# Performance work log

Measured on AMD Instinct MI355X. Metric: run time of the kernel, lower is better.

## Reference

```python
import jax, jax.numpy as jnp
import numpy as np

N_NODES = 100000
N_EDGES = 1200000
IN_DIM = 64
HID = 64
N_GRAPHS = 512
N_CLASSES = 1
LN_EPS = 1e-5
NORM_EPS = 1e-12


def _layer_norm(x, g, b):
    mu = x.mean(-1, keepdims=True)
    var = ((x - mu) ** 2).mean(-1, keepdims=True)
    return (x - mu) * jax.lax.rsqrt(var + LN_EPS) * g + b


def setup_inputs() -> dict:
    key = jax.random.key(0)
    ks = jax.random.split(key, 20)
    h = jax.random.normal(ks[0], (N_NODES, IN_DIM), jnp.float32)
    src = jax.random.randint(ks[1], (N_EDGES,), 0, N_NODES)
    dst = jax.random.randint(ks[2], (N_EDGES,), 0, N_NODES)
    graph_ids = jnp.sort(jax.random.randint(ks[3], (N_NODES,), 0, N_GRAPHS))
    s1 = 1.0 / np.sqrt(IN_DIM)
    s2 = 1.0 / np.sqrt(HID)
    s3 = 1.0 / np.sqrt(2 * HID)
    return {
        "h": h, "src": src, "dst": dst, "graph_ids": graph_ids,
        "W1": jax.random.normal(ks[4], (IN_DIM, HID), jnp.float32) * s1,
        "b1": jnp.zeros((HID,), jnp.float32),
        "W2": jax.random.normal(ks[5], (HID, HID), jnp.float32) * s2,
        "b2": jnp.zeros((HID,), jnp.float32),
        "g1": jnp.ones((HID,), jnp.float32), "be1": jnp.zeros((HID,), jnp.float32),
        "g2": jnp.ones((HID,), jnp.float32), "be2": jnp.zeros((HID,), jnp.float32),
        "g3": jnp.ones((HID,), jnp.float32), "be3": jnp.zeros((HID,), jnp.float32),
        "g4": jnp.ones((HID,), jnp.float32), "be4": jnp.zeros((HID,), jnp.float32),
        "Wc1": jax.random.normal(ks[6], (2 * HID, HID), jnp.float32) * s3,
        "bc1": jnp.zeros((HID,), jnp.float32),
        "Wc2": jax.random.normal(ks[7], (HID, HID), jnp.float32) * s2,
        "bc2": jnp.zeros((HID,), jnp.float32),
        "Wc3": jax.random.normal(ks[8], (HID, N_CLASSES), jnp.float32) * s2,
        "bc3": jnp.zeros((N_CLASSES,), jnp.float32),
    }


def reference(h, src, dst, graph_ids, W1, b1, W2, b2, g1, be1, g2, be2,
              g3, be3, g4, be4, Wc1, bc1, Wc2, bc2, Wc3, bc3):
    N = N_NODES
    ones_e = jnp.ones((src.shape[0],), jnp.float32)
    # DGL GraphConv norm='both': symmetric degree normalization (clamp 0 -> 1)
    deg_out = jnp.clip(jax.ops.segment_sum(ones_e, src, num_segments=N), 1.0)
    deg_in = jnp.clip(jax.ops.segment_sum(ones_e, dst, num_segments=N), 1.0)
    ns = (deg_out ** -0.5)[:, None]
    nd = (deg_in ** -0.5)[:, None]

    def conv(x, W, b):
        msg = (x * ns)[src]                                  # [E, d] gather
        agg = jax.ops.segment_sum(msg, dst, num_segments=N)  # [N, d] scatter-add
        return (agg * nd) @ W + b

    h1 = jax.nn.relu(_layer_norm(conv(h, W1, b1), g1, be1))
    h1 = jax.nn.relu(_layer_norm(conv(h1, W2, b2), g2, be2))

    # per-graph mean / max pooling (dgl.mean_nodes / dgl.max_nodes)
    ssum = jax.ops.segment_sum(h1, graph_ids, num_segments=N_GRAPHS)
    cnt = jnp.clip(jax.ops.segment_sum(jnp.ones((N,), jnp.float32), graph_ids,
                                       num_segments=N_GRAPHS), 1.0)
    hg = ssum / cnt[:, None]
    hg_max = jax.ops.segment_max(h1, graph_ids, num_segments=N_GRAPHS)

    def l2norm(x):  # F.normalize(p=2, dim=1)
        n = jnp.sqrt((x * x).sum(-1, keepdims=True))
        return x / jnp.maximum(n, NORM_EPS)

    hg = jnp.concatenate([l2norm(hg), l2norm(hg_max)], axis=1)  # [G, 2*HID]
    out = jax.nn.relu(_layer_norm(hg @ Wc1 + bc1, g3, be3))
    out = jax.nn.relu(_layer_norm(out @ Wc2 + bc2, g4, be4))
    return out @ Wc3 + bc3
```

## Files before the change

kernel.cpp:

```cpp
#include <hip/hip_runtime.h>
#include <math.h>

#define HID 64
#define LN_EPS 1e-5f
#define NORM_EPS 1e-12f
#define CHUNK 1024
#define CONV_BLOCKS 2048

__device__ __forceinline__ float wave_sum64(float v) {
#pragma unroll
    for (int o = 32; o > 0; o >>= 1) v += __shfl_xor(v, o, 64);
    return v;
}

__device__ __forceinline__ int lower_bound_dev(const int* __restrict__ a, int n, int key) {
    int lo = 0, hi = n;
    while (lo < hi) {
        int mid = (lo + hi) >> 1;
        if (a[mid] < key) lo = mid + 1; else hi = mid;
    }
    return lo;
}

__global__ __launch_bounds__(256) void count_kernel(const int* __restrict__ src,
                                                    const int* __restrict__ dst,
                                                    int* __restrict__ cnt_out,
                                                    int* __restrict__ cnt_in,
                                                    int E) {
    int e0 = (blockIdx.x * 256 + threadIdx.x) * 4;
    if (e0 + 3 < E) {
        int4 s4 = *reinterpret_cast<const int4*>(src + e0);
        int4 d4 = *reinterpret_cast<const int4*>(dst + e0);
        atomicAdd(&cnt_out[s4.x], 1); atomicAdd(&cnt_out[s4.y], 1);
        atomicAdd(&cnt_out[s4.z], 1); atomicAdd(&cnt_out[s4.w], 1);
        atomicAdd(&cnt_in[d4.x], 1);  atomicAdd(&cnt_in[d4.y], 1);
        atomicAdd(&cnt_in[d4.z], 1);  atomicAdd(&cnt_in[d4.w], 1);
    } else {
        for (int e = e0; e < E; ++e) {
            atomicAdd(&cnt_out[src[e]], 1);
            atomicAdd(&cnt_in[dst[e]], 1);
        }
    }
}

__global__ __launch_bounds__(256) void scan1_kernel(const int* __restrict__ cnt_in,
                                                    const int* __restrict__ cnt_out,
                                                    float* __restrict__ ns,
                                                    float* __restrict__ nd,
                                                    int* __restrict__ cs,
                                                    int* __restrict__ partials,
                                                    int N) {
    __shared__ int wsum[4];
    int t = threadIdx.x;
    int lane = t & 63, wave = t >> 6;
    int base = blockIdx.x * CHUNK + t * 4;
    int v0 = (base + 0 < N) ? cnt_in[base + 0] : 0;
    int v1 = (base + 1 < N) ? cnt_in[base + 1] : 0;
    int v2 = (base + 2 < N) ? cnt_in[base + 2] : 0;
    int v3 = (base + 3 < N) ? cnt_in[base + 3] : 0;

    if (base + 3 < N) {
        int4 co = *reinterpret_cast<const int4*>(cnt_out + base);
        float4 nsv = make_float4(rsqrtf((float)max(co.x, 1)), rsqrtf((float)max(co.y, 1)),
                                 rsqrtf((float)max(co.z, 1)), rsqrtf((float)max(co.w, 1)));
        float4 ndv = make_float4(rsqrtf((float)max(v0, 1)), rsqrtf((float)max(v1, 1)),
                                 rsqrtf((float)max(v2, 1)), rsqrtf((float)max(v3, 1)));
        *reinterpret_cast<float4*>(ns + base) = nsv;
        *reinterpret_cast<float4*>(nd + base) = ndv;
    } else {
        for (int i = base; i < N; ++i) {
            ns[i] = rsqrtf((float)max(cnt_out[i], 1));
            nd[i] = rsqrtf((float)max(cnt_in[i], 1));
        }
    }

    int tsum = v0 + v1 + v2 + v3;
    int x = tsum;
#pragma unroll
    for (int off = 1; off < 64; off <<= 1) {
        int y = __shfl_up(x, off, 64);
        if (lane >= off) x += y;
    }
    if (lane == 63) wsum[wave] = x;
    __syncthreads();
    int waveoff = 0;
    for (int w = 0; w < wave; ++w) waveoff += wsum[w];
    int off0 = waveoff + x - tsum;
    if (base + 0 < N) cs[base + 0] = off0;
    if (base + 1 < N) cs[base + 1] = off0 + v0;
    if (base + 2 < N) cs[base + 2] = off0 + v0 + v1;
    if (base + 3 < N) cs[base + 3] = off0 + v0 + v1 + v2;
    if (t == 255) partials[blockIdx.x] = waveoff + x;
}

__global__ __launch_bounds__(256) void scan2_kernel(int* __restrict__ partials, int nch) {
    __shared__ int wsum[4];
    int t = threadIdx.x;
    int lane = t & 63, wave = t >> 6;
    int base = t * 4;
    int v0 = (base + 0 < nch) ? partials[base + 0] : 0;
    int v1 = (base + 1 < nch) ? partials[base + 1] : 0;
    int v2 = (base + 2 < nch) ? partials[base + 2] : 0;
    int v3 = (base + 3 < nch) ? partials[base + 3] : 0;
    int tsum = v0 + v1 + v2 + v3;
    int x = tsum;
#pragma unroll
    for (int off = 1; off < 64; off <<= 1) {
        int y = __shfl_up(x, off, 64);
        if (lane >= off) x += y;
    }
    if (lane == 63) wsum[wave] = x;
    __syncthreads();
    int waveoff = 0;
    for (int w = 0; w < wave; ++w) waveoff += wsum[w];
    int off0 = waveoff + x - tsum;
    if (base + 0 < nch) partials[base + 0] = off0;
    if (base + 1 < nch) partials[base + 1] = off0 + v0;
    if (base + 2 < nch) partials[base + 2] = off0 + v0 + v1;
    if (base + 3 < nch) partials[base + 3] = off0 + v0 + v1 + v2;
}

__global__ __launch_bounds__(256) void scan3_kernel(int* __restrict__ cs,
                                                    const int* __restrict__ partials,
                                                    int* __restrict__ cursor,
                                                    int N, int E) {
    int n = blockIdx.x * 256 + threadIdx.x;
    if (n < N) {
        int v = cs[n] + partials[n / CHUNK];
        cs[n] = v;
        cursor[n] = v;
    }
    if (n == 0) cs[N] = E;
}

__global__ __launch_bounds__(256) void fill_kernel(const int* __restrict__ src,
                                                   const int* __restrict__ dst,
                                                   const float* __restrict__ ns,
                                                   int* __restrict__ cursor,
                                                   int2* __restrict__ epack,
                                                   int E) {
    int e0 = (blockIdx.x * 256 + threadIdx.x) * 4;
    if (e0 + 3 < E) {
        int4 s4 = *reinterpret_cast<const int4*>(src + e0);
        int4 d4 = *reinterpret_cast<const int4*>(dst + e0);
        float w0 = ns[s4.x], w1 = ns[s4.y], w2 = ns[s4.z], w3 = ns[s4.w];
        int p0 = atomicAdd(&cursor[d4.x], 1);
        int p1 = atomicAdd(&cursor[d4.y], 1);
        int p2 = atomicAdd(&cursor[d4.z], 1);
        int p3 = atomicAdd(&cursor[d4.w], 1);
        epack[p0] = make_int2(s4.x, __float_as_int(w0));
        epack[p1] = make_int2(s4.y, __float_as_int(w1));
        epack[p2] = make_int2(s4.z, __float_as_int(w2));
        epack[p3] = make_int2(s4.w, __float_as_int(w3));
    } else {
        for (int e = e0; e < E; ++e) {
            int s = src[e], d = dst[e];
            int p = atomicAdd(&cursor[d], 1);
            epack[p] = make_int2(s, __float_as_int(ns[s]));
        }
    }
}

__global__ __launch_bounds__(256, 8) void conv_kernel(const float* __restrict__ x,
                                                      const int2* __restrict__ epack,
                                                      const int* __restrict__ cs,
                                                      const float* __restrict__ nd,
                                                      const float* __restrict__ W,
                                                      const float* __restrict__ b,
                                                      const float* __restrict__ gam,
                                                      const float* __restrict__ bet,
                                                      float* __restrict__ out,
                                                      int N) {
    __shared__ float Ws[HID * HID];
    int tid = threadIdx.x;
#pragma unroll
    for (int i = tid; i < HID * HID / 4; i += 256) {
        reinterpret_cast<float4*>(Ws)[i] = reinterpret_cast<const float4*>(W)[i];
    }
    __syncthreads();
    int wave = tid >> 6;
    int lane = tid & 63;
    float bl = b[lane], gl = gam[lane], bel = bet[lane];

    for (int n = blockIdx.x * 4 + wave; n < N; n += CONV_BLOCKS * 4) {
        int beg = cs[n], end = cs[n + 1];
        float ndv = nd[n];
        float acc = 0.0f;
        int e = beg;
        for (; e + 4 <= end; e += 4) {
            int2 p0 = epack[e + 0];
            int2 p1 = epack[e + 1];
            int2 p2 = epack[e + 2];
            int2 p3 = epack[e + 3];
            float v0 = x[(size_t)p0.x * HID + lane];
            float v1 = x[(size_t)p1.x * HID + lane];
            float v2 = x[(size_t)p2.x * HID + lane];
            float v3 = x[(size_t)p3.x * HID + lane];
            acc = fmaf(v0, __int_as_float(p0.y), acc);
            acc = fmaf(v1, __int_as_float(p1.y), acc);
            acc = fmaf(v2, __int_as_float(p2.y), acc);
            acc = fmaf(v3, __int_as_float(p3.y), acc);
        }
        for (; e < end; ++e) {
            int2 p = epack[e];
            acc = fmaf(x[(size_t)p.x * HID + lane], __int_as_float(p.y), acc);
        }
        float t = acc * ndv;

        float y = bl;
#pragma unroll 8
        for (int k = 0; k < HID; ++k) {
            y = fmaf(__shfl(t, k, 64), Ws[k * HID + lane], y);
        }
        float mu = wave_sum64(y) * (1.0f / HID);
        float d = y - mu;
        float var = wave_sum64(d * d) * (1.0f / HID);
        float o = d * rsqrtf(var + LN_EPS) * gl + bel;
        o = fmaxf(o, 0.0f);
        out[(size_t)n * HID + lane] = o;
    }
}

__global__ __launch_bounds__(256) void pool_kernel(const float* __restrict__ h1,
                                                   const int* __restrict__ gid,
                                                   float* __restrict__ gsum,
                                                   float* __restrict__ gmaxf,
                                                   float* __restrict__ gcnt,
                                                   int N) {
    __shared__ float psum[4][HID];
    __shared__ float pmax[4][HID];
    __shared__ int se[2];
    int g = blockIdx.x;
    int tid = threadIdx.x;
    if (tid == 0) se[0] = lower_bound_dev(gid, N, g);
    if (tid == 64) se[1] = lower_bound_dev(gid, N, g + 1);
    __syncthreads();
    int s = se[0], e = se[1];
    int wave = tid >> 6, lane = tid & 63;
    float sum = 0.0f, mx = 0.0f;
    for (int r = s + wave; r < e; r += 4) {
        float v = h1[(size_t)r * HID + lane];
        sum += v;
        mx = fmaxf(mx, v);
    }
    psum[wave][lane] = sum;
    pmax[wave][lane] = mx;
    __syncthreads();
    if (tid < HID) {
        float ts = psum[0][tid] + psum[1][tid] + psum[2][tid] + psum[3][tid];
        float tm = fmaxf(fmaxf(pmax[0][tid], pmax[1][tid]), fmaxf(pmax[2][tid], pmax[3][tid]));
        gsum[(size_t)g * HID + tid] = ts;
        gmaxf[(size_t)g * HID + tid] = tm;
        if (tid == 0) gcnt[g] = (float)(e - s);
    }
}

__global__ __launch_bounds__(64) void head_kernel(const float* __restrict__ gsum,
                                                  const float* __restrict__ gmaxf,
                                                  const float* __restrict__ gcnt,
                                                  const float* __restrict__ Wc1,
                                                  const float* __restrict__ bc1,
                                                  const float* __restrict__ g3,
                                                  const float* __restrict__ be3,
                                                  const float* __restrict__ Wc2,
                                                  const float* __restrict__ bc2,
                                                  const float* __restrict__ g4,
                                                  const float* __restrict__ be4,
                                                  const float* __restrict__ Wc3,
                                                  const float* __restrict__ bc3,
                                                  float* __restrict__ out) {
    __shared__ float hg[2 * HID];
    __shared__ float t1[HID];
    int g = blockIdx.x;
    int lane = threadIdx.x;

    float cnt = fmaxf(gcnt[g], 1.0f);
    float mean = gsum[(size_t)g * HID + lane] / cnt;
    float mx = gmaxf[(size_t)g * HID + lane];

    float s1 = sqrtf(wave_sum64(mean * mean));
    float a = mean / fmaxf(s1, NORM_EPS);
    float s2 = sqrtf(wave_sum64(mx * mx));
    float bmx = mx / fmaxf(s2, NORM_EPS);

    hg[lane] = a;
    hg[HID + lane] = bmx;
    __syncthreads();

    float y = bc1[lane];
#pragma unroll 8
    for (int k = 0; k < 2 * HID; ++k) {
        y = fmaf(hg[k], Wc1[k * HID + lane], y);
    }
    float mu = wave_sum64(y) * (1.0f / HID);
    float d = y - mu;
    float var = wave_sum64(d * d) * (1.0f / HID);
    float o = d * rsqrtf(var + LN_EPS) * g3[lane] + be3[lane];
    o = fmaxf(o, 0.0f);
    t1[lane] = o;
    __syncthreads();

    float y2 = bc2[lane];
#pragma unroll 8
    for (int k = 0; k < HID; ++k) {
        y2 = fmaf(t1[k], Wc2[k * HID + lane], y2);
    }
    mu = wave_sum64(y2) * (1.0f / HID);
    d = y2 - mu;
    var = wave_sum64(d * d) * (1.0f / HID);
    o = d * rsqrtf(var + LN_EPS) * g4[lane] + be4[lane];
    o = fmaxf(o, 0.0f);

    float v = o * Wc3[lane];
    v = wave_sum64(v);
    if (lane == 0) out[g] = v + bc3[0];
}

extern "C" void kernel_launch(void* const* d_in, const int* in_sizes, int n_in,
                              void* d_out, int out_size, void* d_ws, size_t ws_size,
                              hipStream_t stream) {
    const float* h   = (const float*)d_in[0];
    const int*   src = (const int*)d_in[1];
    const int*   dst = (const int*)d_in[2];
    const int*   gid = (const int*)d_in[3];
    const float* W1  = (const float*)d_in[4];
    const float* b1  = (const float*)d_in[5];
    const float* W2  = (const float*)d_in[6];
    const float* b2  = (const float*)d_in[7];
    const float* g1  = (const float*)d_in[8];
    const float* be1 = (const float*)d_in[9];
    const float* g2  = (const float*)d_in[10];
    const float* be2 = (const float*)d_in[11];
    const float* g3  = (const float*)d_in[12];
    const float* be3 = (const float*)d_in[13];
    const float* g4  = (const float*)d_in[14];
    const float* be4 = (const float*)d_in[15];
    const float* Wc1 = (const float*)d_in[16];
    const float* bc1 = (const float*)d_in[17];
    const float* Wc2 = (const float*)d_in[18];
    const float* bc2 = (const float*)d_in[19];
    const float* Wc3 = (const float*)d_in[20];
    const float* bc3 = (const float*)d_in[21];
    float* out = (float*)d_out;

    const int N = in_sizes[0] / HID;
    const int E = in_sizes[1];
    const int G = out_size;

    char* ws = (char*)d_ws;
    float* h1     = (float*)ws;
    float* h2     = h1 + (size_t)N * HID;
    int2*  epack  = (int2*)(h2 + (size_t)N * HID);
    float* ns     = (float*)(epack + E);
    float* nd     = ns + N;
    int*   cnt_out= (int*)(nd + N);
    int*   cnt_in = cnt_out + N;
    int*   cs     = cnt_in + N;
    int*   partials = cs + N + 4;
    float* gsum   = (float*)(partials + 1024);
    float* gmaxf  = gsum + (size_t)G * HID;
    float* gcnt   = gmaxf + (size_t)G * HID;

    const int nch = (N + CHUNK - 1) / CHUNK;
    const int E4 = (E + 3) / 4;

    hipMemsetAsync(cnt_out, 0, sizeof(int) * (size_t)2 * N, stream);

    count_kernel<<<(E4 + 255) / 256, 256, 0, stream>>>(src, dst, cnt_out, cnt_in, E);
    scan1_kernel<<<nch, 256, 0, stream>>>(cnt_in, cnt_out, ns, nd, cs, partials, N);
    scan2_kernel<<<1, 256, 0, stream>>>(partials, nch);
    scan3_kernel<<<(N + 255) / 256, 256, 0, stream>>>(cs, partials, cnt_out, N, E);
    fill_kernel<<<(E4 + 255) / 256, 256, 0, stream>>>(src, dst, ns, cnt_out, epack, E);

    conv_kernel<<<CONV_BLOCKS, 256, 0, stream>>>(h, epack, cs, nd, W1, b1, g1, be1, h1, N);
    conv_kernel<<<CONV_BLOCKS, 256, 0, stream>>>(h1, epack, cs, nd, W2, b2, g2, be2, h2, N);

    pool_kernel<<<G, 256, 0, stream>>>(h2, gid, gsum, gmaxf, gcnt, N);

    head_kernel<<<G, 64, 0, stream>>>(gsum, gmaxf, gcnt, Wc1, bc1, g3, be3,
                                      Wc2, bc2, g4, be4, Wc3, bc3, out);
}
```

Measured before the change: 595.9 us.

## Gather fp16 prescaled node features and drop per-edge weights from CSR

Source-degree normalization is folded into the node features ahead of time: a new prescale kernel for layer 1, and the layer-1 conv epilogue for layer 2. Features are stored as fp16, which halves the bytes moved per gathered row. The edge array shrinks from int2 (index plus weight) to a plain int index, and the inner loop becomes plain adds. This cuts gather bandwidth and CSR traffic, at the cost of fp16 rounding error in the aggregated features and one extra elementwise kernel launch.

```diff
diff --git a/kernel.cpp b/kernel.cpp
--- a/kernel.cpp
+++ b/kernel.cpp
@@ -6,6 +6,8 @@
 #define NORM_EPS 1e-12f
 #define CHUNK 1024
 #define CONV_BLOCKS 2048
+
+typedef _Float16 half4v __attribute__((ext_vector_type(4)));
 
 __device__ __forceinline__ float wave_sum64(float v) {
 #pragma unroll
@@ -133,43 +135,58 @@
     if (n == 0) cs[N] = E;
 }
 
+__global__ __launch_bounds__(256) void prescale_kernel(const float* __restrict__ x,
+                                                       const float* __restrict__ ns,
+                                                       _Float16* __restrict__ xs,
+                                                       int total) {
+    int i = (blockIdx.x * 256 + threadIdx.x) * 4;
+    if (i >= total) return;
+    float w = ns[i >> 6];
+    float4 v = *reinterpret_cast<const float4*>(x + i);
+    half4v o;
+    o.x = (_Float16)(v.x * w);
+    o.y = (_Float16)(v.y * w);
+    o.z = (_Float16)(v.z * w);
+    o.w = (_Float16)(v.w * w);
+    *reinterpret_cast<half4v*>(xs + i) = o;
+}
+
 __global__ __launch_bounds__(256) void fill_kernel(const int* __restrict__ src,
                                                    const int* __restrict__ dst,
-                                                   const float* __restrict__ ns,
                                                    int* __restrict__ cursor,
-                                                   int2* __restrict__ epack,
+                                                   int* __restrict__ eidx,
                                                    int E) {
     int e0 = (blockIdx.x * 256 + threadIdx.x) * 4;
     if (e0 + 3 < E) {
         int4 s4 = *reinterpret_cast<const int4*>(src + e0);
         int4 d4 = *reinterpret_cast<const int4*>(dst + e0);
-        float w0 = ns[s4.x], w1 = ns[s4.y], w2 = ns[s4.z], w3 = ns[s4.w];
         int p0 = atomicAdd(&cursor[d4.x], 1);
         int p1 = atomicAdd(&cursor[d4.y], 1);
         int p2 = atomicAdd(&cursor[d4.z], 1);
         int p3 = atomicAdd(&cursor[d4.w], 1);
-        epack[p0] = make_int2(s4.x, __float_as_int(w0));
-        epack[p1] = make_int2(s4.y, __float_as_int(w1));
-        epack[p2] = make_int2(s4.z, __float_as_int(w2));
-        epack[p3] = make_int2(s4.w, __float_as_int(w3));
+        eidx[p0] = s4.x;
+        eidx[p1] = s4.y;
+        eidx[p2] = s4.z;
+        eidx[p3] = s4.w;
     } else {
         for (int e = e0; e < E; ++e) {
-            int s = src[e], d = dst[e];
-            int p = atomicAdd(&cursor[d], 1);
-            epack[p] = make_int2(s, __float_as_int(ns[s]));
-        }
-    }
-}
-
-__global__ __launch_bounds__(256, 8) void conv_kernel(const float* __restrict__ x,
-                                                      const int2* __restrict__ epack,
+            int p = atomicAdd(&cursor[dst[e]], 1);
+            eidx[p] = src[e];
+        }
+    }
+}
+
+template <int MODE>
+__global__ __launch_bounds__(256, 8) void conv_kernel(const _Float16* __restrict__ xs,
+                                                      const int* __restrict__ eidx,
                                                       const int* __restrict__ cs,
                                                       const float* __restrict__ nd,
+                                                      const float* __restrict__ ns,
                                                       const float* __restrict__ W,
                                                       const float* __restrict__ b,
                                                       const float* __restrict__ gam,
                                                       const float* __restrict__ bet,
-                                                      float* __restrict__ out,
+                                                      void* __restrict__ outp,
                                                       int N) {
     __shared__ float Ws[HID * HID];
     int tid = threadIdx.x;
@@ -184,28 +201,23 @@
 
     for (int n = blockIdx.x * 4 + wave; n < N; n += CONV_BLOCKS * 4) {
         int beg = cs[n], end = cs[n + 1];
-        float ndv = nd[n];
         float acc = 0.0f;
         int e = beg;
         for (; e + 4 <= end; e += 4) {
-            int2 p0 = epack[e + 0];
-            int2 p1 = epack[e + 1];
-            int2 p2 = epack[e + 2];
-            int2 p3 = epack[e + 3];
-            float v0 = x[(size_t)p0.x * HID + lane];
-            float v1 = x[(size_t)p1.x * HID + lane];
-            float v2 = x[(size_t)p2.x * HID + lane];
-            float v3 = x[(size_t)p3.x * HID + lane];
-            acc = fmaf(v0, __int_as_float(p0.y), acc);
-            acc = fmaf(v1, __int_as_float(p1.y), acc);
-            acc = fmaf(v2, __int_as_float(p2.y), acc);
-            acc = fmaf(v3, __int_as_float(p3.y), acc);
+            int s0 = eidx[e + 0];
+            int s1 = eidx[e + 1];
+            int s2 = eidx[e + 2];
+            int s3 = eidx[e + 3];
+            float v0 = (float)xs[(size_t)s0 * HID + lane];
+            float v1 = (float)xs[(size_t)s1 * HID + lane];
+            float v2 = (float)xs[(size_t)s2 * HID + lane];
+            float v3 = (float)xs[(size_t)s3 * HID + lane];
+            acc += (v0 + v1) + (v2 + v3);
         }
         for (; e < end; ++e) {
-            int2 p = epack[e];
-            acc = fmaf(x[(size_t)p.x * HID + lane], __int_as_float(p.y), acc);
-        }
-        float t = acc * ndv;
+            acc += (float)xs[(size_t)eidx[e] * HID + lane];
+        }
+        float t = acc * nd[n];
 
         float y = bl;
 #pragma unroll 8
@@ -217,7 +229,11 @@
         float var = wave_sum64(d * d) * (1.0f / HID);
         float o = d * rsqrtf(var + LN_EPS) * gl + bel;
         o = fmaxf(o, 0.0f);
-        out[(size_t)n * HID + lane] = o;
+        if (MODE == 1) {
+            ((_Float16*)outp)[(size_t)n * HID + lane] = (_Float16)(o * ns[n]);
+        } else {
+            ((float*)outp)[(size_t)n * HID + lane] = o;
+        }
     }
 }
 
@@ -348,10 +364,11 @@
     const int G = out_size;
 
     char* ws = (char*)d_ws;
-    float* h1     = (float*)ws;
-    float* h2     = h1 + (size_t)N * HID;
-    int2*  epack  = (int2*)(h2 + (size_t)N * HID);
-    float* ns     = (float*)(epack + E);
+    _Float16* xs1 = (_Float16*)ws;
+    _Float16* xs2 = xs1 + (size_t)N * HID;
+    float* h2     = (float*)(xs2 + (size_t)N * HID);
+    int*   eidx   = (int*)(h2 + (size_t)N * HID);
+    float* ns     = (float*)(eidx + E);
     float* nd     = ns + N;
     int*   cnt_out= (int*)(nd + N);
     int*   cnt_in = cnt_out + N;
@@ -363,6 +380,7 @@
 
     const int nch = (N + CHUNK - 1) / CHUNK;
     const int E4 = (E + 3) / 4;
+    const int total = N * HID;
 
     hipMemsetAsync(cnt_out, 0, sizeof(int) * (size_t)2 * N, stream);
 
@@ -370,10 +388,11 @@
     scan1_kernel<<<nch, 256, 0, stream>>>(cnt_in, cnt_out, ns, nd, cs, partials, N);
     scan2_kernel<<<1, 256, 0, stream>>>(partials, nch);
     scan3_kernel<<<(N + 255) / 256, 256, 0, stream>>>(cs, partials, cnt_out, N, E);
-    fill_kernel<<<(E4 + 255) / 256, 256, 0, stream>>>(src, dst, ns, cnt_out, epack, E);
-
-    conv_kernel<<<CONV_BLOCKS, 256, 0, stream>>>(h, epack, cs, nd, W1, b1, g1, be1, h1, N);
-    conv_kernel<<<CONV_BLOCKS, 256, 0, stream>>>(h1, epack, cs, nd, W2, b2, g2, be2, h2, N);
+    prescale_kernel<<<(total / 4 + 255) / 256, 256, 0, stream>>>(h, ns, xs1, total);
+    fill_kernel<<<(E4 + 255) / 256, 256, 0, stream>>>(src, dst, cnt_out, eidx, E);
+
+    conv_kernel<1><<<CONV_BLOCKS, 256, 0, stream>>>(xs1, eidx, cs, nd, ns, W1, b1, g1, be1, xs2, N);
+    conv_kernel<0><<<CONV_BLOCKS, 256, 0, stream>>>(xs2, eidx, cs, nd, ns, W2, b2, g2, be2, h2, N);
 
     pool_kernel<<<G, 256, 0, stream>>>(h2, gid, gsum, gmaxf, gcnt, N);
 
```

Result: faster. 577.2 us (-3.1%).
